# Kernel optimization log

Hardware: AMD Instinct MI355X
Metric: run time of the kernel (lower is better)

The kernel has to match this reference:

```python
import jax, jax.numpy as jnp
import numpy as np

HEADS = 16
DIM_HEAD = 64
CLAMP = 50.0


def _mh_rmsnorm(x, gamma):
    # x: [b, h, n, d], gamma: [h, 1, d]; F.normalize(dim=-1) * gamma * sqrt(d)
    norm = jnp.linalg.norm(x, axis=-1, keepdims=True)
    return x / jnp.maximum(norm, 1e-12) * gamma * (DIM_HEAD ** 0.5)


def _proj_qkv(x, W):
    # x: [b, n, d_in], W: [d_in, 3*h*dh] -> q,k,v each [b, h, n, dh]
    b, n, _ = x.shape
    qkv = (x @ W).reshape(b, n, 3, HEADS, DIM_HEAD)
    qkv = jnp.transpose(qkv, (2, 0, 3, 1, 4))  # [3, b, h, n, dh]
    return qkv[0], qkv[1], qkv[2]


def setup_inputs() -> dict:
    key = jax.random.key(0)
    ks = jax.random.split(key, 12)
    d1, d2 = 1024, 768
    dim_inner = HEADS * DIM_HEAD
    x1 = jax.random.normal(ks[0], (1, 3072, d1), dtype=jnp.float32)
    x2 = jax.random.normal(ks[1], (1, 1024, d2), dtype=jnp.float32)
    mask1 = jnp.ones((1, 3072), dtype=bool)
    mask2 = jnp.ones((1, 1024), dtype=bool)
    Wqkv1 = jax.random.normal(ks[2], (d1, 3 * dim_inner), dtype=jnp.float32) * (d1 ** -0.5)
    Wqkv2 = jax.random.normal(ks[3], (d2, 3 * dim_inner), dtype=jnp.float32) * (d2 ** -0.5)
    Wout1 = jax.random.normal(ks[4], (dim_inner, d1), dtype=jnp.float32) * (dim_inner ** -0.5)
    Wout2 = jax.random.normal(ks[5], (dim_inner, d2), dtype=jnp.float32) * (dim_inner ** -0.5)
    qg1 = jnp.ones((HEADS, 1, DIM_HEAD), dtype=jnp.float32)
    kg1 = jnp.ones((HEADS, 1, DIM_HEAD), dtype=jnp.float32)
    qg2 = jnp.ones((HEADS, 1, DIM_HEAD), dtype=jnp.float32)
    kg2 = jnp.ones((HEADS, 1, DIM_HEAD), dtype=jnp.float32)
    return dict(x1=x1, x2=x2, mask1=mask1, mask2=mask2,
                Wqkv1=Wqkv1, Wqkv2=Wqkv2, Wout1=Wout1, Wout2=Wout2,
                qg1=qg1, kg1=kg1, qg2=qg2, kg2=kg2)


def reference(x1, x2, mask1, mask2, Wqkv1, Wqkv2, Wout1, Wout2, qg1, kg1, qg2, kg2):
    n1 = x1.shape[1]
    q1, k1, v1 = _proj_qkv(x1, Wqkv1)
    q2, k2, v2 = _proj_qkv(x2, Wqkv2)
    # per-modality multi-head RMSNorm on q and k
    q1, k1 = _mh_rmsnorm(q1, qg1), _mh_rmsnorm(k1, kg1)
    q2, k2 = _mh_rmsnorm(q2, qg2), _mh_rmsnorm(k2, kg2)
    # pack along sequence: [b, h, N, dh]
    q = jnp.concatenate([q1, q2], axis=2)
    k = jnp.concatenate([k1, k2], axis=2)
    v = jnp.concatenate([v1, v2], axis=2)
    mask = jnp.concatenate([mask1, mask2], axis=1)  # [b, N]
    sim = jnp.einsum('bhid,bhjd->bhij', q, k) * (DIM_HEAD ** -0.5)
    sim = jnp.tanh(sim / CLAMP) * CLAMP  # softclamp
    neg = -jnp.finfo(sim.dtype).max
    sim = jnp.where(mask[:, None, None, :], sim, neg)
    attn = jax.nn.softmax(sim, axis=-1)
    out = jnp.einsum('bhij,bhjd->bhid', attn, v)
    b, h, N, dh = out.shape
    out = jnp.transpose(out, (0, 2, 1, 3)).reshape(b, N, h * dh)  # merge heads
    out1 = out[:, :n1] @ Wout1
    out2 = out[:, n1:] @ Wout2
    return (out1, out2)
```

## Files before the change

kernel.cpp:

```cpp
#include <hip/hip_runtime.h>
#include <hip/hip_bf16.h>
#include <math.h>

#define HEADS 16
#define DH 64
#define N1 3072
#define N2 1024
#define NTOT 4096
#define D1 1024
#define D2 768
#define DINNER 1024

typedef __attribute__((ext_vector_type(8))) short bf16x8;
typedef __attribute__((ext_vector_type(16))) float f32x16;

__device__ __forceinline__ unsigned short f2bf(float x) {
    unsigned u = __float_as_uint(x);
    return (unsigned short)((u + 0x7fffu + ((u >> 16) & 1u)) >> 16);
}

#define GLL16(gsrc, ldst)                                                     \
    __builtin_amdgcn_global_load_lds(                                         \
        (const __attribute__((address_space(1))) unsigned int*)(gsrc),        \
        (__attribute__((address_space(3))) unsigned int*)(ldst), 16, 0, 0)

__global__ __launch_bounds__(256) void convert_split(
    const float* __restrict__ in, ushort* __restrict__ hi, ushort* __restrict__ lo)
{
    int idx = blockIdx.x * 256 + threadIdx.x;
    float4 x = reinterpret_cast<const float4*>(in)[idx];
    float xs[4] = {x.x, x.y, x.z, x.w};
    ushort4 h4, l4;
#pragma unroll
    for (int i = 0; i < 4; i++) {
        unsigned short hb = f2bf(xs[i]);
        float hf = __uint_as_float(((unsigned)hb) << 16);
        ((unsigned short*)&h4)[i] = hb;
        ((unsigned short*)&l4)[i] = f2bf(xs[i] - hf);
    }
    reinterpret_cast<ushort4*>(hi)[idx] = h4;
    reinterpret_cast<ushort4*>(lo)[idx] = l4;
}

__global__ __launch_bounds__(256) void convert_split_t(
    const float* __restrict__ in, ushort* __restrict__ hiT, ushort* __restrict__ loT,
    int K, int N)
{
    __shared__ float Ls[32][33];
    const int tid = threadIdx.x;
    const int kt = blockIdx.y, nt = blockIdx.x;
    {
        int r = tid >> 3, c4 = (tid & 7) * 4;
        float4 x = *reinterpret_cast<const float4*>(
            &in[(size_t)(kt * 32 + r) * N + nt * 32 + c4]);
        Ls[r][c4 + 0] = x.x; Ls[r][c4 + 1] = x.y;
        Ls[r][c4 + 2] = x.z; Ls[r][c4 + 3] = x.w;
    }
    __syncthreads();
    {
        int nl = tid >> 3, k4 = (tid & 7) * 4;
        ushort4 h4, l4;
#pragma unroll
        for (int i = 0; i < 4; i++) {
            float x = Ls[k4 + i][nl];
            unsigned short hb = f2bf(x);
            float hf = __uint_as_float(((unsigned)hb) << 16);
            ((unsigned short*)&h4)[i] = hb;
            ((unsigned short*)&l4)[i] = f2bf(x - hf);
        }
        size_t o = (size_t)(nt * 32 + nl) * K + kt * 32 + k4;
        *reinterpret_cast<ushort4*>(&hiT[o]) = h4;
        *reinterpret_cast<ushort4*>(&loT[o]) = l4;
    }
}

template <bool SCATTER>
__device__ __forceinline__ void gemm_body(
    bf16x8 (&LA)[2][4][2][64], bf16x8 (&LB)[2][4][2][64],
    const ushort* __restrict__ Ah, const ushort* __restrict__ Al,
    const ushort* __restrict__ Bh, const ushort* __restrict__ Bl,
    int bx, int by, int M, int N, int K,
    float* __restrict__ C, int ldc,
    float* __restrict__ qb, float* __restrict__ kb, float* __restrict__ vb,
    int n_off)
{
    const int tid = threadIdx.x;
    const int lane = tid & 63;
    const int w = tid >> 6;
    const int wm = w >> 1, wn = w & 1;
    const int row0 = by * 128;
    const int col0 = bx * 128;
    const int half = lane >> 5;

    const size_t aoff = (size_t)(row0 + w * 32 + (lane & 31)) * K + half * 8;
    const size_t boff = (size_t)(col0 + w * 32 + (lane & 31)) * K + half * 8;
    const ushort* pAh = Ah + aoff;
    const ushort* pAl = Al + aoff;
    const ushort* pBh = Bh + boff;
    const ushort* pBl = Bl + boff;

    f32x16 acc[2][2];
#pragma unroll
    for (int mi = 0; mi < 2; mi++)
#pragma unroll
        for (int ni = 0; ni < 2; ni++)
#pragma unroll
            for (int j = 0; j < 16; j++) acc[mi][ni][j] = 0.f;

    for (int k0 = 0; k0 < K; k0 += 32) {
        GLL16(pAh + k0,      &LA[0][w][0][0]);
        GLL16(pAh + k0 + 16, &LA[0][w][1][0]);
        GLL16(pAl + k0,      &LA[1][w][0][0]);
        GLL16(pAl + k0 + 16, &LA[1][w][1][0]);
        GLL16(pBh + k0,      &LB[0][w][0][0]);
        GLL16(pBh + k0 + 16, &LB[0][w][1][0]);
        GLL16(pBl + k0,      &LB[1][w][0][0]);
        GLL16(pBl + k0 + 16, &LB[1][w][1][0]);
        __syncthreads();

#pragma unroll
        for (int ks = 0; ks < 2; ks++) {
            bf16x8 a_h[2], a_l[2], b_h[2], b_l[2];
#pragma unroll
            for (int mi = 0; mi < 2; mi++) {
                a_h[mi] = LA[0][2 * wm + mi][ks][lane];
                a_l[mi] = LA[1][2 * wm + mi][ks][lane];
            }
#pragma unroll
            for (int ni = 0; ni < 2; ni++) {
                b_h[ni] = LB[0][2 * wn + ni][ks][lane];
                b_l[ni] = LB[1][2 * wn + ni][ks][lane];
            }
#pragma unroll
            for (int mi = 0; mi < 2; mi++)
#pragma unroll
                for (int ni = 0; ni < 2; ni++) {
                    acc[mi][ni] = __builtin_amdgcn_mfma_f32_32x32x16_bf16(
                        a_h[mi], b_h[ni], acc[mi][ni], 0, 0, 0);
                    acc[mi][ni] = __builtin_amdgcn_mfma_f32_32x32x16_bf16(
                        a_h[mi], b_l[ni], acc[mi][ni], 0, 0, 0);
                    acc[mi][ni] = __builtin_amdgcn_mfma_f32_32x32x16_bf16(
                        a_l[mi], b_h[ni], acc[mi][ni], 0, 0, 0);
                }
        }
        __syncthreads();
    }

#pragma unroll
    for (int mi = 0; mi < 2; mi++)
#pragma unroll
        for (int ni = 0; ni < 2; ni++) {
            if (!SCATTER) {
                int cb = col0 + wn * 64 + ni * 32 + (lane & 31);
#pragma unroll
                for (int j = 0; j < 16; j++) {
                    int ro = (j & 3) + 8 * (j >> 2) + 4 * half;
                    int rr = row0 + wm * 64 + mi * 32 + ro;
                    C[(size_t)rr * ldc + cb] = acc[mi][ni][j];
                }
            } else {
                int cbase = col0 + wn * 64 + ni * 32;
                int s = cbase >> 10;
                int hh = (cbase >> 6) & 15;
                int dbase = cbase & 63;
                float* basep = (s == 0) ? qb : ((s == 1) ? kb : vb);
#pragma unroll
                for (int j = 0; j < 16; j++) {
                    int ro = (j & 3) + 8 * (j >> 2) + 4 * half;
                    int rr = n_off + row0 + wm * 64 + mi * 32 + ro;
                    basep[((size_t)hh * NTOT + rr) * DH + dbase + (lane & 31)] =
                        acc[mi][ni][j];
                }
            }
        }
}

__global__ __launch_bounds__(256) void gemm_qkv(
    const ushort* x1h, const ushort* x1l, const ushort* w1h, const ushort* w1l,
    const ushort* x2h, const ushort* x2l, const ushort* w2h, const ushort* w2l,
    float* qb, float* kb, float* vb)
{
    __shared__ bf16x8 LA[2][4][2][64];
    __shared__ bf16x8 LB[2][4][2][64];
    int bid = blockIdx.x;
    if (bid < 576) {
        gemm_body<true>(LA, LB, x1h, x1l, w1h, w1l, bid % 24, bid / 24,
                        N1, 3 * DINNER, D1, nullptr, 0, qb, kb, vb, 0);
    } else {
        int b = bid - 576;
        gemm_body<true>(LA, LB, x2h, x2l, w2h, w2l, b % 24, b / 24,
                        N2, 3 * DINNER, D2, nullptr, 0, qb, kb, vb, N1);
    }
}

__global__ __launch_bounds__(256) void gemm_out(
    const ushort* ah, const ushort* al, const ushort* o1h, const ushort* o1l,
    const ushort* o2h, const ushort* o2l, float* out)
{
    __shared__ bf16x8 LA[2][4][2][64];
    __shared__ bf16x8 LB[2][4][2][64];
    int bid = blockIdx.x;
    if (bid < 192) {
        gemm_body<false>(LA, LB, ah, al, o1h, o1l, bid % 8, bid / 8,
                         N1, D1, DINNER, out, D1, nullptr, nullptr, nullptr, 0);
    } else {
        int b = bid - 192;
        gemm_body<false>(LA, LB, ah + (size_t)N1 * DINNER, al + (size_t)N1 * DINNER,
                         o2h, o2l, b % 6, b / 6,
                         N2, D2, DINNER, out + (size_t)N1 * D1, D2,
                         nullptr, nullptr, nullptr, 0);
    }
}

__global__ __launch_bounds__(256) void rmsnorm_qk(
    float* __restrict__ q, float* __restrict__ k,
    const float* __restrict__ qg1, const float* __restrict__ kg1,
    const float* __restrict__ qg2, const float* __restrict__ kg2)
{
    int wid = (blockIdx.x * 256 + threadIdx.x) >> 6;
    int lane = threadIdx.x & 63;
    int which = wid >> 16;
    int rem = wid & 65535;
    int h = rem >> 12;
    int n = rem & 4095;

    float* base = which ? k : q;
    float* p = &base[((size_t)h * NTOT + n) * DH + lane];
    float vv = *p;
    float ss = vv * vv;
#pragma unroll
    for (int m = 1; m < 64; m <<= 1) ss += __shfl_xor(ss, m, 64);
    float norm = sqrtf(ss);
    const float* g = which ? (n < N1 ? kg1 : kg2) : (n < N1 ? qg1 : qg2);
    float gv = g[h * DH + lane];
    *p = vv / fmaxf(norm, 1e-12f) * gv * 8.0f;
}

__global__ __launch_bounds__(256) void prep_kv(
    const float* __restrict__ k, const float* __restrict__ v,
    bf16x8* __restrict__ kvg)
{
    int idx = blockIdx.x * 256 + threadIdx.x;
    int e = idx & 63;
    int pslot = (idx >> 6) & 15;
    int t = (idx >> 10) & 63;
    int h = idx >> 16;
    size_t base = ((size_t)h * 64 + t) * 32;

    bf16x8 hi, lo;
    if (pslot < 8) {
        int kb = pslot >> 2, s = pslot & 3;
        int key = kb * 32 + (e & 31);
        int d = s * 16 + (e >> 5) * 8;
        const float* src = &k[((size_t)h * NTOT + t * 64 + key) * DH + d];
        float4 a = *reinterpret_cast<const float4*>(src);
        float4 b = *reinterpret_cast<const float4*>(src + 4);
        float xs[8] = {a.x, a.y, a.z, a.w, b.x, b.y, b.z, b.w};
#pragma unroll
        for (int j = 0; j < 8; j++) {
            unsigned short hb = f2bf(xs[j]);
            float hf = __uint_as_float(((unsigned)hb) << 16);
            hi[j] = (short)hb;
            lo[j] = (short)f2bf(xs[j] - hf);
        }
        kvg[(base + pslot) * 64 + e] = hi;
        kvg[(base + 8 + pslot) * 64 + e] = lo;
    } else {
        int qs = pslot - 8;
        int db = qs >> 2, ks = qs & 3;
        int d = db * 32 + (e & 31);
        int k0 = ks * 16 + (e >> 5) * 8;
#pragma unroll
        for (int j = 0; j < 8; j++) {
            float vv = v[((size_t)h * NTOT + t * 64 + k0 + j) * DH + d];
            unsigned short hb = f2bf(vv);
            float hf = __uint_as_float(((unsigned)hb) << 16);
            hi[j] = (short)hb;
            lo[j] = (short)f2bf(vv - hf);
        }
        kvg[(base + 16 + qs) * 64 + e] = hi;
        kvg[(base + 24 + qs) * 64 + e] = lo;
    }
}

__global__ __launch_bounds__(256) void attn_mfma(
    const float* __restrict__ q, const bf16x8* __restrict__ kvg,
    float* __restrict__ att)
{
    __shared__ bf16x8 TILE[2][32][64];

    const int tid = threadIdx.x;
    const int lane = tid & 63;
    const int w = tid >> 6;
    const int h = blockIdx.y;
    const int qb = blockIdx.x;
    const size_t hbase = (size_t)h * NTOT;
    const int half = lane >> 5;

    bf16x8 qhi[4], qlo[4];
    {
        int row = qb * 128 + w * 32 + (lane & 31);
        const float* qp = &q[(hbase + row) * DH + half * 8];
#pragma unroll
        for (int s = 0; s < 4; s++) {
            float4 a = *reinterpret_cast<const float4*>(qp + s * 16);
            float4 b = *reinterpret_cast<const float4*>(qp + s * 16 + 4);
            float xs[8] = {a.x, a.y, a.z, a.w, b.x, b.y, b.z, b.w};
#pragma unroll
            for (int j = 0; j < 8; j++) {
                float xv = xs[j] * 0.125f;
                unsigned short hb = f2bf(xv);
                float hf = __uint_as_float(((unsigned)hb) << 16);
                qhi[s][j] = (short)hb;
                qlo[s][j] = (short)f2bf(xv - hf);
            }
        }
    }

    auto STAGE = [&](int buf, int t) {
        const bf16x8* gp = kvg + ((size_t)h * 64 + t) * (32 * 64)
                         + (w * 8) * 64 + lane;
#pragma unroll
        for (int i = 0; i < 8; i++)
            GLL16(gp + i * 64, &TILE[buf][w * 8 + i][0]);
    };

    f32x16 o0, o1;
#pragma unroll
    for (int r = 0; r < 16; r++) { o0[r] = 0.f; o1[r] = 0.f; }
    float m = -1e30f, l = 0.f;

    STAGE(0, 0);
    int cur = 0;
    for (int t = 0; t < NTOT / 64; t++) {
        __syncthreads();
        if (t + 1 < NTOT / 64) STAGE(cur ^ 1, t + 1);

        f32x16 S[2];
#pragma unroll
        for (int kb = 0; kb < 2; kb++) {
            f32x16 acc;
#pragma unroll
            for (int r = 0; r < 16; r++) acc[r] = 0.f;
#pragma unroll
            for (int s = 0; s < 4; s++) {
                bf16x8 kh = TILE[cur][kb * 4 + s][lane];
                bf16x8 kl = TILE[cur][8 + kb * 4 + s][lane];
                acc = __builtin_amdgcn_mfma_f32_32x32x16_bf16(kh, qhi[s], acc, 0, 0, 0);
                acc = __builtin_amdgcn_mfma_f32_32x32x16_bf16(kh, qlo[s], acc, 0, 0, 0);
                acc = __builtin_amdgcn_mfma_f32_32x32x16_bf16(kl, qhi[s], acc, 0, 0, 0);
            }
            S[kb] = acc;
        }

        float tmax = -1e30f;
#pragma unroll
        for (int kb = 0; kb < 2; kb++)
#pragma unroll
            for (int r = 0; r < 16; r++) {
                float sv = S[kb][r];
                float x2 = sv * sv * 4e-4f;
                sv = sv * (1.f + x2 * (-0.33333333f +
                           x2 * (0.13333333f - x2 * 0.05396825f)));
                S[kb][r] = sv;
                tmax = fmaxf(tmax, sv);
            }
        tmax = fmaxf(tmax, __shfl_xor(tmax, 32));
        if (__any(tmax > m + 8.f)) {
            float mn = fmaxf(m, tmax);
            float sc = __expf(m - mn);
            m = mn;
            l *= sc;
#pragma unroll
            for (int j = 0; j < 16; j++) {
                int ro = (j & 3) + 8 * (j >> 2) + half * 4;
                float scj = __shfl(sc, ro);
                o0[j] *= scj;
                o1[j] *= scj;
            }
        }
        float psum = 0.f;
#pragma unroll
        for (int kb = 0; kb < 2; kb++)
#pragma unroll
            for (int r = 0; r < 16; r++) {
                float p = __expf(S[kb][r] - m);
                S[kb][r] = p;
                psum += p;
            }
        l += psum + __shfl_xor(psum, 32);

#pragma unroll
        for (int ks = 0; ks < 4; ks++) {
            unsigned vh[2][2], vl[2][2];
#pragma unroll
            for (int j8 = 0; j8 < 2; j8++)
#pragma unroll
                for (int tt = 0; tt < 2; tt++) {
                    const int g = 2 * ks + j8;
                    const int kb = g >> 2;
                    const int rl = 2 * tt + (g & 3) * 4;
                    float p0 = S[kb][rl], p1 = S[kb][rl + 1];
                    unsigned hd;
                    asm("v_cvt_pk_bf16_f32 %0, %1, %2" : "=v"(hd) : "v"(p0), "v"(p1));
                    float h0 = __uint_as_float(hd << 16);
                    float h1 = __uint_as_float(hd & 0xffff0000u);
                    float r0 = p0 - h0, r1 = p1 - h1;
                    unsigned ldw;
                    asm("v_cvt_pk_bf16_f32 %0, %1, %2" : "=v"(ldw) : "v"(r0), "v"(r1));
                    vh[j8][tt] = hd;
                    vl[j8][tt] = ldw;
                }
            bool lo32 = (half == 0);
            unsigned a0 = (unsigned)__shfl_xor((int)vh[1][0], 32);
            unsigned a1 = (unsigned)__shfl_xor((int)vh[1][1], 32);
            unsigned b0 = (unsigned)__shfl_xor((int)vh[0][0], 32);
            unsigned b1 = (unsigned)__shfl_xor((int)vh[0][1], 32);
            unsigned c0 = (unsigned)__shfl_xor((int)vl[1][0], 32);
            unsigned c1 = (unsigned)__shfl_xor((int)vl[1][1], 32);
            unsigned d0 = (unsigned)__shfl_xor((int)vl[0][0], 32);
            unsigned d1 = (unsigned)__shfl_xor((int)vl[0][1], 32);
            union { unsigned u[4]; bf16x8 vv; } PH, PL;
            PH.u[0] = lo32 ? vh[0][0] : a0;
            PH.u[1] = lo32 ? vh[0][1] : a1;
            PH.u[2] = lo32 ? b0 : vh[1][0];
            PH.u[3] = lo32 ? b1 : vh[1][1];
            PL.u[0] = lo32 ? vl[0][0] : c0;
            PL.u[1] = lo32 ? vl[0][1] : c1;
            PL.u[2] = lo32 ? d0 : vl[1][0];
            PL.u[3] = lo32 ? d1 : vl[1][1];

            {
                bf16x8 vbh = TILE[cur][16 + ks][lane];
                bf16x8 vbl = TILE[cur][24 + ks][lane];
                o0 = __builtin_amdgcn_mfma_f32_32x32x16_bf16(PH.vv, vbh, o0, 0, 0, 0);
                o0 = __builtin_amdgcn_mfma_f32_32x32x16_bf16(PL.vv, vbh, o0, 0, 0, 0);
                o0 = __builtin_amdgcn_mfma_f32_32x32x16_bf16(PH.vv, vbl, o0, 0, 0, 0);
            }
            {
                bf16x8 vbh = TILE[cur][20 + ks][lane];
                bf16x8 vbl = TILE[cur][28 + ks][lane];
                o1 = __builtin_amdgcn_mfma_f32_32x32x16_bf16(PH.vv, vbh, o1, 0, 0, 0);
                o1 = __builtin_amdgcn_mfma_f32_32x32x16_bf16(PL.vv, vbh, o1, 0, 0, 0);
                o1 = __builtin_amdgcn_mfma_f32_32x32x16_bf16(PH.vv, vbl, o1, 0, 0, 0);
            }
        }
        cur ^= 1;
    }

#pragma unroll
    for (int j = 0; j < 16; j++) {
        int ro = (j & 3) + 8 * (j >> 2) + half * 4;
        float lj = __shfl(l, ro);
        float inv = 1.f / lj;
        int row = qb * 128 + w * 32 + ro;
        att[(size_t)row * DINNER + h * DH + (lane & 31)] = o0[j] * inv;
        att[(size_t)row * DINNER + h * DH + 32 + (lane & 31)] = o1[j] * inv;
    }
}

extern "C" void kernel_launch(void* const* d_in, const int* in_sizes, int n_in,
                              void* d_out, int out_size, void* d_ws, size_t ws_size,
                              hipStream_t stream)
{
    const float* x1    = (const float*)d_in[0];
    const float* x2    = (const float*)d_in[1];
    const float* Wqkv1 = (const float*)d_in[4];
    const float* Wqkv2 = (const float*)d_in[5];
    const float* Wout1 = (const float*)d_in[6];
    const float* Wout2 = (const float*)d_in[7];
    const float* qg1   = (const float*)d_in[8];
    const float* kg1   = (const float*)d_in[9];
    const float* qg2   = (const float*)d_in[10];
    const float* kg2   = (const float*)d_in[11];
    float* out = (float*)d_out;

    float* ws = (float*)d_ws;
    const size_t HQ = (size_t)HEADS * NTOT * DH;
    float* q   = ws;
    float* k   = q + HQ;
    float* v   = k + HQ;
    float* att = v + HQ;

    ushort* x1h = (ushort*)(att + (size_t)NTOT * DINNER);
    ushort* x1l = x1h + (size_t)N1 * D1;
    ushort* x2h = x1l + (size_t)N1 * D1;
    ushort* x2l = x2h + (size_t)N2 * D2;
    ushort* w1h = x2l + (size_t)N2 * D2;
    ushort* w1l = w1h + (size_t)3 * DINNER * D1;
    ushort* w2h = w1l + (size_t)3 * DINNER * D1;
    ushort* w2l = w2h + (size_t)3 * DINNER * D2;
    ushort* o1h = w2l + (size_t)3 * DINNER * D2;
    ushort* o1l = o1h + (size_t)DINNER * D1;
    ushort* o2h = o1l + (size_t)DINNER * D1;
    ushort* o2l = o2h + (size_t)D2 * DINNER;
    bf16x8* kvg = (bf16x8*)x1h;
    ushort* atth = x1h;
    ushort* attl = w1h;

    dim3 blk(256);

    convert_split_t<<<dim3(96, 32), blk, 0, stream>>>(Wqkv1, w1h, w1l, D1, 3 * DINNER);
    convert_split_t<<<dim3(96, 24), blk, 0, stream>>>(Wqkv2, w2h, w2l, D2, 3 * DINNER);
    convert_split_t<<<dim3(32, 32), blk, 0, stream>>>(Wout1, o1h, o1l, DINNER, D1);
    convert_split_t<<<dim3(24, 32), blk, 0, stream>>>(Wout2, o2h, o2l, DINNER, D2);
    convert_split<<<dim3(3072), blk, 0, stream>>>(x1, x1h, x1l);
    convert_split<<<dim3(768), blk, 0, stream>>>(x2, x2h, x2l);

    gemm_qkv<<<dim3(768), blk, 0, stream>>>(
        x1h, x1l, w1h, w1l, x2h, x2l, w2h, w2l, q, k, v);

    rmsnorm_qk<<<dim3(32768), blk, 0, stream>>>(q, k, qg1, kg1, qg2, kg2);

    prep_kv<<<dim3(4096), blk, 0, stream>>>(k, v, kvg);

    attn_mfma<<<dim3(NTOT / 128, HEADS), blk, 0, stream>>>(q, kvg, att);

    convert_split<<<dim3(4096), blk, 0, stream>>>(att, atth, attl);
    gemm_out<<<dim3(240), blk, 0, stream>>>(
        atth, attl, o1h, o1l, o2h, o2l, out);
}
```

Measured before the change: 561.0 us.

## Double-buffer GEMM LDS, fuse attention output split, merge conversion launches, add setprio

The GEMM body now double-buffers its LDS tiles, so the global-to-LDS copy of the next K slice is issued while MFMAs run on the current slice. This also drops one barrier per iteration. The attention kernel writes its output directly as bf16 hi/lo pairs, which removes a separate conversion pass over the attention output. The six weight and input conversion launches are merged into two. s_setprio hints are added around the MFMA sections in attention. LDS use per GEMM block doubles, and atth/attl now alias the att buffer region.

```diff
diff --git a/kernel.cpp b/kernel.cpp
--- a/kernel.cpp
+++ b/kernel.cpp
@@ -24,10 +24,17 @@
         (const __attribute__((address_space(1))) unsigned int*)(gsrc),        \
         (__attribute__((address_space(3))) unsigned int*)(ldst), 16, 0, 0)
 
-__global__ __launch_bounds__(256) void convert_split(
-    const float* __restrict__ in, ushort* __restrict__ hi, ushort* __restrict__ lo)
-{
-    int idx = blockIdx.x * 256 + threadIdx.x;
+__global__ __launch_bounds__(256) void convert_x(
+    const float* __restrict__ x1, ushort* __restrict__ x1h, ushort* __restrict__ x1l,
+    const float* __restrict__ x2, ushort* __restrict__ x2h, ushort* __restrict__ x2l)
+{
+    int bid = blockIdx.x;
+    const float* in;
+    ushort *hi, *lo;
+    int idx;
+    if (bid < 3072) { in = x1; hi = x1h; lo = x1l; idx = bid * 256 + threadIdx.x; }
+    else { in = x2; hi = x2h; lo = x2l; idx = (bid - 3072) * 256 + threadIdx.x; }
+
     float4 x = reinterpret_cast<const float4*>(in)[idx];
     float xs[4] = {x.x, x.y, x.z, x.w};
     ushort4 h4, l4;
@@ -42,13 +49,23 @@
     reinterpret_cast<ushort4*>(lo)[idx] = l4;
 }
 
-__global__ __launch_bounds__(256) void convert_split_t(
-    const float* __restrict__ in, ushort* __restrict__ hiT, ushort* __restrict__ loT,
-    int K, int N)
+__global__ __launch_bounds__(256) void convert_wT(
+    const float* __restrict__ W1, ushort* __restrict__ w1h, ushort* __restrict__ w1l,
+    const float* __restrict__ W2, ushort* __restrict__ w2h, ushort* __restrict__ w2l,
+    const float* __restrict__ O1, ushort* __restrict__ o1h, ushort* __restrict__ o1l,
+    const float* __restrict__ O2, ushort* __restrict__ o2h, ushort* __restrict__ o2l)
 {
     __shared__ float Ls[32][33];
     const int tid = threadIdx.x;
-    const int kt = blockIdx.y, nt = blockIdx.x;
+    int bid = blockIdx.x;
+    const float* in;
+    ushort *hiT, *loT;
+    int K, N, nt, kt;
+    if (bid < 3072)      { in = W1; hiT = w1h; loT = w1l; K = D1;     N = 3 * DINNER; nt = bid % 96; kt = bid / 96; }
+    else if (bid < 5376) { int b = bid - 3072; in = W2; hiT = w2h; loT = w2l; K = D2;     N = 3 * DINNER; nt = b % 96; kt = b / 96; }
+    else if (bid < 6400) { int b = bid - 5376; in = O1; hiT = o1h; loT = o1l; K = DINNER; N = D1;         nt = b % 32; kt = b / 32; }
+    else                 { int b = bid - 6400; in = O2; hiT = o2h; loT = o2l; K = DINNER; N = D2;         nt = b % 24; kt = b / 24; }
+
     {
         int r = tid >> 3, c4 = (tid & 7) * 4;
         float4 x = *reinterpret_cast<const float4*>(
@@ -76,7 +93,7 @@
 
 template <bool SCATTER>
 __device__ __forceinline__ void gemm_body(
-    bf16x8 (&LA)[2][4][2][64], bf16x8 (&LB)[2][4][2][64],
+    bf16x8 (&LA)[2][2][4][2][64], bf16x8 (&LB)[2][2][4][2][64],
     const ushort* __restrict__ Ah, const ushort* __restrict__ Al,
     const ushort* __restrict__ Bh, const ushort* __restrict__ Bl,
     int bx, int by, int M, int N, int K,
@@ -99,6 +116,17 @@
     const ushort* pBh = Bh + boff;
     const ushort* pBl = Bl + boff;
 
+    auto STAGE = [&](int buf, int k0) {
+        GLL16(pAh + k0,      &LA[buf][0][w][0][0]);
+        GLL16(pAh + k0 + 16, &LA[buf][0][w][1][0]);
+        GLL16(pAl + k0,      &LA[buf][1][w][0][0]);
+        GLL16(pAl + k0 + 16, &LA[buf][1][w][1][0]);
+        GLL16(pBh + k0,      &LB[buf][0][w][0][0]);
+        GLL16(pBh + k0 + 16, &LB[buf][0][w][1][0]);
+        GLL16(pBl + k0,      &LB[buf][1][w][0][0]);
+        GLL16(pBl + k0 + 16, &LB[buf][1][w][1][0]);
+    };
+
     f32x16 acc[2][2];
 #pragma unroll
     for (int mi = 0; mi < 2; mi++)
@@ -107,29 +135,24 @@
 #pragma unroll
             for (int j = 0; j < 16; j++) acc[mi][ni][j] = 0.f;
 
+    STAGE(0, 0);
+    int cur = 0;
     for (int k0 = 0; k0 < K; k0 += 32) {
-        GLL16(pAh + k0,      &LA[0][w][0][0]);
-        GLL16(pAh + k0 + 16, &LA[0][w][1][0]);
-        GLL16(pAl + k0,      &LA[1][w][0][0]);
-        GLL16(pAl + k0 + 16, &LA[1][w][1][0]);
-        GLL16(pBh + k0,      &LB[0][w][0][0]);
-        GLL16(pBh + k0 + 16, &LB[0][w][1][0]);
-        GLL16(pBl + k0,      &LB[1][w][0][0]);
-        GLL16(pBl + k0 + 16, &LB[1][w][1][0]);
         __syncthreads();
+        if (k0 + 32 < K) STAGE(cur ^ 1, k0 + 32);
 
 #pragma unroll
         for (int ks = 0; ks < 2; ks++) {
             bf16x8 a_h[2], a_l[2], b_h[2], b_l[2];
 #pragma unroll
             for (int mi = 0; mi < 2; mi++) {
-                a_h[mi] = LA[0][2 * wm + mi][ks][lane];
-                a_l[mi] = LA[1][2 * wm + mi][ks][lane];
+                a_h[mi] = LA[cur][0][2 * wm + mi][ks][lane];
+                a_l[mi] = LA[cur][1][2 * wm + mi][ks][lane];
             }
 #pragma unroll
             for (int ni = 0; ni < 2; ni++) {
-                b_h[ni] = LB[0][2 * wn + ni][ks][lane];
-                b_l[ni] = LB[1][2 * wn + ni][ks][lane];
+                b_h[ni] = LB[cur][0][2 * wn + ni][ks][lane];
+                b_l[ni] = LB[cur][1][2 * wn + ni][ks][lane];
             }
 #pragma unroll
             for (int mi = 0; mi < 2; mi++)
@@ -143,7 +166,7 @@
                         a_l[mi], b_h[ni], acc[mi][ni], 0, 0, 0);
                 }
         }
-        __syncthreads();
+        cur ^= 1;
     }
 
 #pragma unroll
@@ -180,8 +203,8 @@
     const ushort* x2h, const ushort* x2l, const ushort* w2h, const ushort* w2l,
     float* qb, float* kb, float* vb)
 {
-    __shared__ bf16x8 LA[2][4][2][64];
-    __shared__ bf16x8 LB[2][4][2][64];
+    __shared__ bf16x8 LA[2][2][4][2][64];
+    __shared__ bf16x8 LB[2][2][4][2][64];
     int bid = blockIdx.x;
     if (bid < 576) {
         gemm_body<true>(LA, LB, x1h, x1l, w1h, w1l, bid % 24, bid / 24,
@@ -197,8 +220,8 @@
     const ushort* ah, const ushort* al, const ushort* o1h, const ushort* o1l,
     const ushort* o2h, const ushort* o2l, float* out)
 {
-    __shared__ bf16x8 LA[2][4][2][64];
-    __shared__ bf16x8 LB[2][4][2][64];
+    __shared__ bf16x8 LA[2][2][4][2][64];
+    __shared__ bf16x8 LB[2][2][4][2][64];
     int bid = blockIdx.x;
     if (bid < 192) {
         gemm_body<false>(LA, LB, ah, al, o1h, o1l, bid % 8, bid / 8,
@@ -285,7 +308,7 @@
 
 __global__ __launch_bounds__(256) void attn_mfma(
     const float* __restrict__ q, const bf16x8* __restrict__ kvg,
-    float* __restrict__ att)
+    ushort* __restrict__ atth, ushort* __restrict__ attl)
 {
     __shared__ bf16x8 TILE[2][32][64];
 
@@ -337,6 +360,7 @@
         if (t + 1 < NTOT / 64) STAGE(cur ^ 1, t + 1);
 
         f32x16 S[2];
+        __builtin_amdgcn_s_setprio(1);
 #pragma unroll
         for (int kb = 0; kb < 2; kb++) {
             f32x16 acc;
@@ -352,6 +376,7 @@
             }
             S[kb] = acc;
         }
+        __builtin_amdgcn_s_setprio(0);
 
         float tmax = -1e30f;
 #pragma unroll
@@ -430,6 +455,7 @@
             PL.u[2] = lo32 ? d0 : vl[1][0];
             PL.u[3] = lo32 ? d1 : vl[1][1];
 
+            __builtin_amdgcn_s_setprio(1);
             {
                 bf16x8 vbh = TILE[cur][16 + ks][lane];
                 bf16x8 vbl = TILE[cur][24 + ks][lane];
@@ -444,6 +470,7 @@
                 o1 = __builtin_amdgcn_mfma_f32_32x32x16_bf16(PL.vv, vbh, o1, 0, 0, 0);
                 o1 = __builtin_amdgcn_mfma_f32_32x32x16_bf16(PH.vv, vbl, o1, 0, 0, 0);
             }
+            __builtin_amdgcn_s_setprio(0);
         }
         cur ^= 1;
     }
@@ -454,8 +481,15 @@
         float lj = __shfl(l, ro);
         float inv = 1.f / lj;
         int row = qb * 128 + w * 32 + ro;
-        att[(size_t)row * DINNER + h * DH + (lane & 31)] = o0[j] * inv;
-        att[(size_t)row * DINNER + h * DH + 32 + (lane & 31)] = o1[j] * inv;
+        size_t base = (size_t)row * DINNER + h * DH + (lane & 31);
+        float v0 = o0[j] * inv;
+        float v1 = o1[j] * inv;
+        unsigned short h0 = f2bf(v0);
+        unsigned short h1 = f2bf(v1);
+        atth[base] = h0;
+        atth[base + 32] = h1;
+        attl[base] = f2bf(v0 - __uint_as_float(((unsigned)h0) << 16));
+        attl[base + 32] = f2bf(v1 - __uint_as_float(((unsigned)h1) << 16));
     }
 }
 
@@ -495,17 +529,14 @@
     ushort* o2h = o1l + (size_t)DINNER * D1;
     ushort* o2l = o2h + (size_t)D2 * DINNER;
     bf16x8* kvg = (bf16x8*)x1h;
-    ushort* atth = x1h;
-    ushort* attl = w1h;
+    ushort* atth = (ushort*)att;
+    ushort* attl = atth + (size_t)NTOT * DINNER;
 
     dim3 blk(256);
 
-    convert_split_t<<<dim3(96, 32), blk, 0, stream>>>(Wqkv1, w1h, w1l, D1, 3 * DINNER);
-    convert_split_t<<<dim3(96, 24), blk, 0, stream>>>(Wqkv2, w2h, w2l, D2, 3 * DINNER);
-    convert_split_t<<<dim3(32, 32), blk, 0, stream>>>(Wout1, o1h, o1l, DINNER, D1);
-    convert_split_t<<<dim3(24, 32), blk, 0, stream>>>(Wout2, o2h, o2l, DINNER, D2);
-    convert_split<<<dim3(3072), blk, 0, stream>>>(x1, x1h, x1l);
-    convert_split<<<dim3(768), blk, 0, stream>>>(x2, x2h, x2l);
+    convert_wT<<<dim3(7168), blk, 0, stream>>>(
+        Wqkv1, w1h, w1l, Wqkv2, w2h, w2l, Wout1, o1h, o1l, Wout2, o2h, o2l);
+    convert_x<<<dim3(3840), blk, 0, stream>>>(x1, x1h, x1l, x2, x2h, x2l);
 
     gemm_qkv<<<dim3(768), blk, 0, stream>>>(
         x1h, x1l, w1h, w1l, x2h, x2l, w2h, w2l, q, k, v);
@@ -514,9 +545,8 @@
 
     prep_kv<<<dim3(4096), blk, 0, stream>>>(k, v, kvg);
 
-    attn_mfma<<<dim3(NTOT / 128, HEADS), blk, 0, stream>>>(q, kvg, att);
-
-    convert_split<<<dim3(4096), blk, 0, stream>>>(att, atth, attl);
+    attn_mfma<<<dim3(NTOT / 128, HEADS), blk, 0, stream>>>(q, kvg, atth, attl);
+
     gemm_out<<<dim3(240), blk, 0, stream>>>(
         atth, attl, o1h, o1l, o2h, o2l, out);
 }
```

Measured after the change: 560.8 us. Within noise of the previous version (-0.0%).
